# Kernel tuning notes

Hardware: AMD Instinct MI355X
Metric: run time of the kernel (lower is better)

## Reference

```python
import jax, jax.numpy as jnp
import numpy as np


def _leaky(x):
    return jnp.where(x >= 0, x, 0.01 * x)  # nn.LeakyReLU default slope


def _conv1x1(x, w):
    # x: [B, C, H, W], w: [O, C] (1x1 conv == per-pixel channel GEMM)
    return jnp.einsum('bchw,oc->bohw', x, w)


def setup_inputs() -> dict:
    key = jax.random.key(0)
    ks = jax.random.split(key, 12)

    def kaiming(k, o, c):  # kaiming_normal_ fan_out, relu gain, 1x1 kernel
        return jax.random.normal(k, (o, c), jnp.float32) * np.float32(np.sqrt(2.0 / o))

    lr_feature = jax.random.normal(ks[0], (1, 32, 256, 512), jnp.float32)
    hr_feature = jax.random.normal(ks[1], (1, 32, 512, 1024), jnp.float32)
    return {
        'lr_feature': lr_feature,
        'hr_feature': hr_feature,
        's1_w0': kaiming(ks[2], 128, 128),
        's1_w1': kaiming(ks[3], 64, 128),
        's1_w2': kaiming(ks[4], 32, 64),
        's1_w3': kaiming(ks[5], 16, 32),
        's1_w4': kaiming(ks[6], 8, 16),
        's1_w5': kaiming(ks[7], 1, 8),
        's2_w0': kaiming(ks[8], 3, 3),
        's2_w1': kaiming(ks[9], 2, 3),
        's2_w2': kaiming(ks[10], 1, 2),
        'fuse_w': jnp.ones((1, 2), jnp.float32),  # fuse weight initialized to 1
    }


def reference(lr_feature, hr_feature, s1_w0, s1_w1, s1_w2, s1_w3, s1_w4, s1_w5,
              s2_w0, s2_w1, s2_w2, fuse_w):
    scale = hr_feature.shape[-1] // lr_feature.shape[-1]  # static python int (=2, even)
    Hh, Wh = hr_feature.shape[-2], hr_feature.shape[-1]

    # nearest-neighbor upsample of lr_feature by `scale` (expand/view trick in torch)
    lr_up = jnp.repeat(jnp.repeat(lr_feature, scale, axis=2), scale, axis=3)

    # representation: [B, 128, Hh, Wh]
    rep = jnp.concatenate(
        [lr_up, hr_feature, lr_up * hr_feature, (lr_up - hr_feature) ** 2], axis=1)

    # similarity_measure1: 1x1-conv MLP chain 128->128->64->32->16->8->1
    o = _leaky(_conv1x1(rep, s1_w0))
    o = _leaky(_conv1x1(o, s1_w1))
    o = _leaky(_conv1x1(o, s1_w2))
    o = _leaky(_conv1x1(o, s1_w3))
    o = _conv1x1(o, s1_w4)
    weights1 = _conv1x1(o, s1_w5)  # [B, 1, Hh, Wh]

    # distance matrix (even-scale branch): 3 channels [dx, dy, norm]
    v = jnp.arange(-(scale // 2), scale // 2 + 1, dtype=jnp.float32)
    m = v.shape[0] // 2
    v = jnp.concatenate([v[:m], v[m + 1:]])  # drop center -> length `scale`
    d0 = jnp.broadcast_to(v[None, :], (scale, scale))
    dm = jnp.stack([d0, d0.T, jnp.sqrt(d0 ** 2 + d0.T ** 2)], axis=0)  # [3,s,s]
    dm = jnp.tile(dm, (1, Hh // scale, Wh // scale))[None]  # [1, 3, Hh, Wh]

    # similarity_measure2: 3->3->2->1
    w2 = _leaky(_conv1x1(dm, s2_w0))
    w2 = _leaky(_conv1x1(w2, s2_w1))
    weights2 = _conv1x1(w2, s2_w2)  # [1, 1, Hh, Wh]

    # fuse (weight forced non-negative via abs, as in forward's .data mutation)
    mapping = _conv1x1(jnp.concatenate([weights1, weights2], axis=1), jnp.abs(fuse_w))
    return mapping
```

## Files before the change

### kernel.cpp

```cpp
#include <hip/hip_runtime.h>

typedef short v8s __attribute__((ext_vector_type(8)));
typedef float v4f __attribute__((ext_vector_type(4)));
typedef unsigned v4u __attribute__((ext_vector_type(4)));

#define Wh   1024
#define Hh   512
#define HWh  (Wh * Hh)
#define Wlr  512
#define HWlr (Wlr * 256)
#define PAD  136
#define ITERS 8
#define NBLK  256

#define WFRAG_SHORTS (53 * 512)
#define ACT_SHORTS   (16 * PAD)
#define LDS_BYTES    ((WFRAG_SHORTS + 16 * ACT_SHORTS) * 2)

__device__ __forceinline__ unsigned short f2bf(float f) {
    union { float f; unsigned u; } v; v.f = f;
    unsigned r = v.u + 0x7FFFu + ((v.u >> 16) & 1u);
    return (unsigned short)(r >> 16);
}
__device__ __forceinline__ unsigned pk2(float a, float b) {
    union { float f; unsigned u; } ua, ub;
    ua.f = a; ub.f = b;
    return __builtin_amdgcn_perm(ub.u + 0x8000u, ua.u + 0x8000u, 0x07060302u);
}
__device__ __forceinline__ float leaky(float x) { return fmaxf(x, 0.01f * x); }

__global__ __launch_bounds__(1024, 4)
void cmfsm_kernel(const float* __restrict__ lr, const float* __restrict__ hr,
                  const float* __restrict__ w0g, const float* __restrict__ w1g,
                  const float* __restrict__ w2g, const float* __restrict__ w3g,
                  const float* __restrict__ w4g, const float* __restrict__ w5g,
                  const float* __restrict__ t0g, const float* __restrict__ t1g,
                  const float* __restrict__ t2g, const float* __restrict__ fwg,
                  float* __restrict__ out)
{
    extern __shared__ unsigned short smem[];
    unsigned short* wfrag = smem;
    unsigned short* actS  = smem + WFRAG_SHORTS;

    const int tid  = threadIdx.x;
    const int lane = tid & 63;
    const int wv   = tid >> 6;
    const int p    = lane & 15;
    const int q    = lane >> 4;

    for (int e = tid; e < 32 * 64; e += 1024) {
        int f = e >> 6, l = e & 63;
        int mt = f >> 2, ks = f & 3, pp = l & 15, qq = l >> 4;
        const float* src = w0g + (mt * 16 + pp) * 128 + ks * 32 + qq * 8;
        unsigned short* dst = wfrag + f * 512 + l * 8;
#pragma unroll
        for (int j = 0; j < 8; ++j) dst[j] = f2bf(src[j]);
    }
    if (tid < 16 * 64) {
        int f = tid >> 6, l = tid & 63;
        int mt = f >> 2, ks = f & 3, pp = l & 15, qq = l >> 4;
        const float* src = w1g + (mt * 16 + pp) * 128 + ks * 32 + qq * 8;
        unsigned short* dst = wfrag + (32 + f) * 512 + l * 8;
#pragma unroll
        for (int j = 0; j < 8; ++j) dst[j] = f2bf(src[j]);
    }
    if (tid < 4 * 64) {
        int f = tid >> 6, l = tid & 63;
        int mt = f >> 1, ks = f & 1, pp = l & 15, qq = l >> 4;
        const float* src = w2g + (mt * 16 + pp) * 64 + ks * 32 + qq * 8;
        unsigned short* dst = wfrag + (48 + f) * 512 + l * 8;
#pragma unroll
        for (int j = 0; j < 8; ++j) dst[j] = f2bf(src[j]);
    }
    if (tid < 64) {
        int l = tid;
        int pp = l & 15, qq = l >> 4;
        const float* src = w3g + pp * 32 + qq * 8;
        unsigned short* dst = wfrag + 52 * 512 + l * 8;
#pragma unroll
        for (int j = 0; j < 8; ++j) dst[j] = f2bf(src[j]);
    }

    float w45[4];
#pragma unroll
    for (int r = 0; r < 4; ++r) {
        float s = 0.f;
#pragma unroll
        for (int j = 0; j < 8; ++j) s += w5g[j] * w4g[j * 16 + q * 4 + r];
        w45[r] = s;
    }

    float w2t0, w2t1, w2t2, w2t3;
    {
        float tab[4];
#pragma unroll
        for (int yp = 0; yp < 2; ++yp)
#pragma unroll
            for (int xp = 0; xp < 2; ++xp) {
                float i0 = xp ? 1.f : -1.f;
                float i1 = yp ? 1.f : -1.f;
                float i2 = 1.41421356237309505f;
                float h0[3], h1[2];
                for (int o = 0; o < 3; ++o)
                    h0[o] = leaky(t0g[o*3+0]*i0 + t0g[o*3+1]*i1 + t0g[o*3+2]*i2);
                for (int o = 0; o < 2; ++o)
                    h1[o] = leaky(t1g[o*3+0]*h0[0] + t1g[o*3+1]*h0[1] + t1g[o*3+2]*h0[2]);
                tab[yp*2+xp] = t2g[0]*h1[0] + t2g[1]*h1[1];
            }
        w2t0 = tab[0]; w2t1 = tab[1]; w2t2 = tab[2]; w2t3 = tab[3];
    }
    const float fa = fabsf(fwg[0]);
    const float fb = fabsf(fwg[1]);

    __syncthreads();

    unsigned short* Arow = actS + wv * ACT_SHORTS + p * PAD;
    const unsigned short* ARq8 = Arow + q * 8;
    unsigned short* AWq4       = Arow + q * 4;
    const unsigned short* WL   = wfrag + lane * 8;

    const float* hrp[8];
    const float* lrp[8];
    {
        const int hbase = blockIdx.x * 2048 + wv * 16 + p;
        const int lbase = blockIdx.x * 512  + wv * 8  + (p >> 1);
#pragma unroll
        for (int j = 0; j < 8; ++j) {
            hrp[j] = hr + (size_t)(q * 8 + j) * HWh  + hbase;
            lrp[j] = lr + (size_t)(q * 8 + j) * HWlr + lbase;
        }
    }

    float h[8], l[8];
#pragma unroll
    for (int j = 0; j < 8; ++j) { h[j] = hrp[j][0]; l[j] = lrp[j][0]; }

#pragma unroll 1
    for (int t = 0; t < 2; ++t) {
#pragma unroll
        for (int s = 0; s < 4; ++s) {
            v4u bf0, bf1, bf2, bf3;
#pragma unroll
            for (int u = 0; u < 4; ++u) {
                float l0 = l[2*u], l1 = l[2*u+1];
                float h0 = h[2*u], h1 = h[2*u+1];
                bf0[u] = pk2(l0, l1);
                bf1[u] = pk2(h0, h1);
                bf2[u] = pk2(l0 * h0, l1 * h1);
                float d0 = l0 - h0, d1 = l1 - h1;
                bf3[u] = pk2(d0 * d0, d1 * d1);
            }
            v8s b0 = __builtin_bit_cast(v8s, bf0);
            v8s b1 = __builtin_bit_cast(v8s, bf1);
            v8s b2 = __builtin_bit_cast(v8s, bf2);
            v8s b3 = __builtin_bit_cast(v8s, bf3);

#pragma unroll
            for (int j = 0; j < 8; ++j) hrp[j] += 256;
            if (t == 0 || s < 3) {
                const int nlr = ((s + 1) & 3) * 128;
#pragma unroll
                for (int j = 0; j < 8; ++j) {
                    h[j] = hrp[j][0];
                    l[j] = lrp[j][nlr];
                }
            }

#pragma unroll
            for (int half = 0; half < 2; ++half) {
                v4f acc[4];
#pragma unroll
                for (int m2 = 0; m2 < 4; ++m2) acc[m2] = (v4f){0.f, 0.f, 0.f, 0.f};
#pragma unroll
                for (int ks = 0; ks < 4; ++ks) {
                    v8s b = (ks == 0) ? b0 : (ks == 1) ? b1 : (ks == 2) ? b2 : b3;
#pragma unroll
                    for (int m2 = 0; m2 < 4; ++m2) {
                        const int mt = half * 4 + m2;
                        v8s a = *(const v8s*)(WL + (mt * 4 + ks) * 512);
                        acc[m2] = __builtin_amdgcn_mfma_f32_16x16x32_bf16(a, b, acc[m2], 0, 0, 0);
                    }
                }
#pragma unroll
                for (int m2 = 0; m2 < 4; ++m2) {
                    const int mt = half * 4 + m2;
                    uint2 v;
                    v.x = pk2(leaky(acc[m2][0]), leaky(acc[m2][1]));
                    v.y = pk2(leaky(acc[m2][2]), leaky(acc[m2][3]));
                    *(uint2*)(AWq4 + mt * 16) = v;
                }
            }

            {
                v4f acc1[4];
#pragma unroll
                for (int mt = 0; mt < 4; ++mt) acc1[mt] = (v4f){0.f, 0.f, 0.f, 0.f};
#pragma unroll
                for (int ks = 0; ks < 4; ++ks) {
                    v8s b = *(const v8s*)(ARq8 + ks * 32);
#pragma unroll
                    for (int mt = 0; mt < 4; ++mt) {
                        v8s a = *(const v8s*)(WL + (32 + mt * 4 + ks) * 512);
                        acc1[mt] = __builtin_amdgcn_mfma_f32_16x16x32_bf16(a, b, acc1[mt], 0, 0, 0);
                    }
                }
#pragma unroll
                for (int mt = 0; mt < 4; ++mt) {
                    uint2 v;
                    v.x = pk2(leaky(acc1[mt][0]), leaky(acc1[mt][1]));
                    v.y = pk2(leaky(acc1[mt][2]), leaky(acc1[mt][3]));
                    *(uint2*)(AWq4 + mt * 16) = v;
                }
            }

            {
                v4f acc2[2];
#pragma unroll
                for (int mt = 0; mt < 2; ++mt) acc2[mt] = (v4f){0.f, 0.f, 0.f, 0.f};
#pragma unroll
                for (int ks = 0; ks < 2; ++ks) {
                    v8s b = *(const v8s*)(ARq8 + ks * 32);
#pragma unroll
                    for (int mt = 0; mt < 2; ++mt) {
                        v8s a = *(const v8s*)(WL + (48 + mt * 2 + ks) * 512);
                        acc2[mt] = __builtin_amdgcn_mfma_f32_16x16x32_bf16(a, b, acc2[mt], 0, 0, 0);
                    }
                }
#pragma unroll
                for (int mt = 0; mt < 2; ++mt) {
                    uint2 v;
                    v.x = pk2(leaky(acc2[mt][0]), leaky(acc2[mt][1]));
                    v.y = pk2(leaky(acc2[mt][2]), leaky(acc2[mt][3]));
                    *(uint2*)(AWq4 + mt * 16) = v;
                }
            }

            {
                v8s b = *(const v8s*)(ARq8);
                v8s a = *(const v8s*)(WL + 52 * 512);
                v4f acc3 = __builtin_amdgcn_mfma_f32_16x16x32_bf16(a, b, (v4f){0.f, 0.f, 0.f, 0.f}, 0, 0, 0);

                float part = 0.f;
#pragma unroll
                for (int r = 0; r < 4; ++r) part += w45[r] * leaky(acc3[r]);
                part += __shfl_xor(part, 16, 64);
                part += __shfl_xor(part, 32, 64);

                if (q == 0) {
                    const float w2v = t ? ((p & 1) ? w2t3 : w2t2)
                                        : ((p & 1) ? w2t1 : w2t0);
                    const int gidx = blockIdx.x * 2048 + (t * 4 + s) * 256 + wv * 16 + p;
                    out[gidx] = fa * part + fb * w2v;
                }
            }
        }
    }
}

extern "C" void kernel_launch(void* const* d_in, const int* in_sizes, int n_in,
                              void* d_out, int out_size, void* d_ws, size_t ws_size,
                              hipStream_t stream) {
    const float* lr  = (const float*)d_in[0];
    const float* hr  = (const float*)d_in[1];
    const float* w0g = (const float*)d_in[2];
    const float* w1g = (const float*)d_in[3];
    const float* w2g = (const float*)d_in[4];
    const float* w3g = (const float*)d_in[5];
    const float* w4g = (const float*)d_in[6];
    const float* w5g = (const float*)d_in[7];
    const float* t0g = (const float*)d_in[8];
    const float* t1g = (const float*)d_in[9];
    const float* t2g = (const float*)d_in[10];
    const float* fwg = (const float*)d_in[11];
    float* out = (float*)d_out;

    hipLaunchKernelGGL(cmfsm_kernel, dim3(NBLK), dim3(1024), LDS_BYTES, stream,
                       lr, hr, w0g, w1g, w2g, w3g, w4g, w5g, t0g, t1g, t2g, fwg, out);
}
```

Measured before the change: 149.6 us.

## Chain MLP layers through registers by permuting weight K-order instead of LDS

Removes the per-wave LDS activation staging buffer. MFMA accumulator outputs are packed directly into the B operands of the next layer, and the weight fragments for layers 1-3 are loaded with a permuted K index so the register layout of the outputs lines up. The layer-3 weight fragment is also hoisted into a register before the loop. This eliminates LDS writes and reads, and the waits between layers, at the cost of more live registers (8 accumulators for layer 0), which could add spill or scheduling pressure.

```diff
diff --git a/kernel.cpp b/kernel.cpp
--- a/kernel.cpp
+++ b/kernel.cpp
@@ -9,13 +9,11 @@
 #define HWh  (Wh * Hh)
 #define Wlr  512
 #define HWlr (Wlr * 256)
-#define PAD  136
 #define ITERS 8
 #define NBLK  256
 
 #define WFRAG_SHORTS (53 * 512)
-#define ACT_SHORTS   (16 * PAD)
-#define LDS_BYTES    ((WFRAG_SHORTS + 16 * ACT_SHORTS) * 2)
+#define LDS_BYTES    (WFRAG_SHORTS * 2)
 
 __device__ __forceinline__ unsigned short f2bf(float f) {
     union { float f; unsigned u; } v; v.f = f;
@@ -28,6 +26,15 @@
     return __builtin_amdgcn_perm(ub.u + 0x8000u, ua.u + 0x8000u, 0x07060302u);
 }
 __device__ __forceinline__ float leaky(float x) { return fmaxf(x, 0.01f * x); }
+
+__device__ __forceinline__ v8s relay(const v4f& e, const v4f& o) {
+    v4u w;
+    w[0] = pk2(leaky(e[0]), leaky(e[1]));
+    w[1] = pk2(leaky(e[2]), leaky(e[3]));
+    w[2] = pk2(leaky(o[0]), leaky(o[1]));
+    w[3] = pk2(leaky(o[2]), leaky(o[3]));
+    return __builtin_bit_cast(v8s, w);
+}
 
 __global__ __launch_bounds__(1024, 4)
 void cmfsm_kernel(const float* __restrict__ lr, const float* __restrict__ hr,
@@ -40,7 +47,6 @@
 {
     extern __shared__ unsigned short smem[];
     unsigned short* wfrag = smem;
-    unsigned short* actS  = smem + WFRAG_SHORTS;
 
     const int tid  = threadIdx.x;
     const int lane = tid & 63;
@@ -59,26 +65,29 @@
     if (tid < 16 * 64) {
         int f = tid >> 6, l = tid & 63;
         int mt = f >> 2, ks = f & 3, pp = l & 15, qq = l >> 4;
-        const float* src = w1g + (mt * 16 + pp) * 128 + ks * 32 + qq * 8;
+        const float* srcrow = w1g + (mt * 16 + pp) * 128;
         unsigned short* dst = wfrag + (32 + f) * 512 + l * 8;
 #pragma unroll
-        for (int j = 0; j < 8; ++j) dst[j] = f2bf(src[j]);
+        for (int j = 0; j < 8; ++j)
+            dst[j] = f2bf(srcrow[ks * 32 + ((j >> 2) << 4) + qq * 4 + (j & 3)]);
     }
     if (tid < 4 * 64) {
         int f = tid >> 6, l = tid & 63;
         int mt = f >> 1, ks = f & 1, pp = l & 15, qq = l >> 4;
-        const float* src = w2g + (mt * 16 + pp) * 64 + ks * 32 + qq * 8;
+        const float* srcrow = w2g + (mt * 16 + pp) * 64;
         unsigned short* dst = wfrag + (48 + f) * 512 + l * 8;
 #pragma unroll
-        for (int j = 0; j < 8; ++j) dst[j] = f2bf(src[j]);
+        for (int j = 0; j < 8; ++j)
+            dst[j] = f2bf(srcrow[ks * 32 + ((j >> 2) << 4) + qq * 4 + (j & 3)]);
     }
     if (tid < 64) {
         int l = tid;
         int pp = l & 15, qq = l >> 4;
-        const float* src = w3g + pp * 32 + qq * 8;
+        const float* srcrow = w3g + pp * 32;
         unsigned short* dst = wfrag + 52 * 512 + l * 8;
 #pragma unroll
-        for (int j = 0; j < 8; ++j) dst[j] = f2bf(src[j]);
+        for (int j = 0; j < 8; ++j)
+            dst[j] = f2bf(srcrow[((j >> 2) << 4) + qq * 4 + (j & 3)]);
     }
 
     float w45[4];
@@ -114,10 +123,7 @@
 
     __syncthreads();
 
-    unsigned short* Arow = actS + wv * ACT_SHORTS + p * PAD;
-    const unsigned short* ARq8 = Arow + q * 8;
-    unsigned short* AWq4       = Arow + q * 4;
-    const unsigned short* WL   = wfrag + lane * 8;
+    const unsigned short* WL = wfrag + lane * 8;
 
     const float* hrp[8];
     const float* lrp[8];
@@ -130,6 +136,8 @@
             lrp[j] = lr + (size_t)(q * 8 + j) * HWlr + lbase;
         }
     }
+
+    const v8s a3 = *(const v8s*)(WL + 52 * 512);
 
     float h[8], l[8];
 #pragma unroll
@@ -166,79 +174,54 @@
                 }
             }
 
-#pragma unroll
-            for (int half = 0; half < 2; ++half) {
-                v4f acc[4];
-#pragma unroll
-                for (int m2 = 0; m2 < 4; ++m2) acc[m2] = (v4f){0.f, 0.f, 0.f, 0.f};
-#pragma unroll
-                for (int ks = 0; ks < 4; ++ks) {
-                    v8s b = (ks == 0) ? b0 : (ks == 1) ? b1 : (ks == 2) ? b2 : b3;
-#pragma unroll
-                    for (int m2 = 0; m2 < 4; ++m2) {
-                        const int mt = half * 4 + m2;
-                        v8s a = *(const v8s*)(WL + (mt * 4 + ks) * 512);
-                        acc[m2] = __builtin_amdgcn_mfma_f32_16x16x32_bf16(a, b, acc[m2], 0, 0, 0);
-                    }
-                }
-#pragma unroll
-                for (int m2 = 0; m2 < 4; ++m2) {
-                    const int mt = half * 4 + m2;
-                    uint2 v;
-                    v.x = pk2(leaky(acc[m2][0]), leaky(acc[m2][1]));
-                    v.y = pk2(leaky(acc[m2][2]), leaky(acc[m2][3]));
-                    *(uint2*)(AWq4 + mt * 16) = v;
+            v4f acc0[8];
+#pragma unroll
+            for (int mt = 0; mt < 8; ++mt) acc0[mt] = (v4f){0.f, 0.f, 0.f, 0.f};
+#pragma unroll
+            for (int ks = 0; ks < 4; ++ks) {
+                v8s b = (ks == 0) ? b0 : (ks == 1) ? b1 : (ks == 2) ? b2 : b3;
+#pragma unroll
+                for (int mt = 0; mt < 8; ++mt) {
+                    v8s a = *(const v8s*)(WL + (mt * 4 + ks) * 512);
+                    acc0[mt] = __builtin_amdgcn_mfma_f32_16x16x32_bf16(a, b, acc0[mt], 0, 0, 0);
+                }
+            }
+
+            v8s c1[4];
+#pragma unroll
+            for (int ks = 0; ks < 4; ++ks) c1[ks] = relay(acc0[2*ks], acc0[2*ks+1]);
+
+            v4f acc1[4];
+#pragma unroll
+            for (int mt = 0; mt < 4; ++mt) acc1[mt] = (v4f){0.f, 0.f, 0.f, 0.f};
+#pragma unroll
+            for (int ks = 0; ks < 4; ++ks) {
+#pragma unroll
+                for (int mt = 0; mt < 4; ++mt) {
+                    v8s a = *(const v8s*)(WL + (32 + mt * 4 + ks) * 512);
+                    acc1[mt] = __builtin_amdgcn_mfma_f32_16x16x32_bf16(a, c1[ks], acc1[mt], 0, 0, 0);
+                }
+            }
+
+            v8s c2[2];
+#pragma unroll
+            for (int ks = 0; ks < 2; ++ks) c2[ks] = relay(acc1[2*ks], acc1[2*ks+1]);
+
+            v4f acc2[2];
+#pragma unroll
+            for (int mt = 0; mt < 2; ++mt) acc2[mt] = (v4f){0.f, 0.f, 0.f, 0.f};
+#pragma unroll
+            for (int ks = 0; ks < 2; ++ks) {
+#pragma unroll
+                for (int mt = 0; mt < 2; ++mt) {
+                    v8s a = *(const v8s*)(WL + (48 + mt * 2 + ks) * 512);
+                    acc2[mt] = __builtin_amdgcn_mfma_f32_16x16x32_bf16(a, c2[ks], acc2[mt], 0, 0, 0);
                 }
             }
 
             {
-                v4f acc1[4];
-#pragma unroll
-                for (int mt = 0; mt < 4; ++mt) acc1[mt] = (v4f){0.f, 0.f, 0.f, 0.f};
-#pragma unroll
-                for (int ks = 0; ks < 4; ++ks) {
-                    v8s b = *(const v8s*)(ARq8 + ks * 32);
-#pragma unroll
-                    for (int mt = 0; mt < 4; ++mt) {
-                        v8s a = *(const v8s*)(WL + (32 + mt * 4 + ks) * 512);
-                        acc1[mt] = __builtin_amdgcn_mfma_f32_16x16x32_bf16(a, b, acc1[mt], 0, 0, 0);
-                    }
-                }
-#pragma unroll
-                for (int mt = 0; mt < 4; ++mt) {
-                    uint2 v;
-                    v.x = pk2(leaky(acc1[mt][0]), leaky(acc1[mt][1]));
-                    v.y = pk2(leaky(acc1[mt][2]), leaky(acc1[mt][3]));
-                    *(uint2*)(AWq4 + mt * 16) = v;
-                }
-            }
-
-            {
-                v4f acc2[2];
-#pragma unroll
-                for (int mt = 0; mt < 2; ++mt) acc2[mt] = (v4f){0.f, 0.f, 0.f, 0.f};
-#pragma unroll
-                for (int ks = 0; ks < 2; ++ks) {
-                    v8s b = *(const v8s*)(ARq8 + ks * 32);
-#pragma unroll
-                    for (int mt = 0; mt < 2; ++mt) {
-                        v8s a = *(const v8s*)(WL + (48 + mt * 2 + ks) * 512);
-                        acc2[mt] = __builtin_amdgcn_mfma_f32_16x16x32_bf16(a, b, acc2[mt], 0, 0, 0);
-                    }
-                }
-#pragma unroll
-                for (int mt = 0; mt < 2; ++mt) {
-                    uint2 v;
-                    v.x = pk2(leaky(acc2[mt][0]), leaky(acc2[mt][1]));
-                    v.y = pk2(leaky(acc2[mt][2]), leaky(acc2[mt][3]));
-                    *(uint2*)(AWq4 + mt * 16) = v;
-                }
-            }
-
-            {
-                v8s b = *(const v8s*)(ARq8);
-                v8s a = *(const v8s*)(WL + 52 * 512);
-                v4f acc3 = __builtin_amdgcn_mfma_f32_16x16x32_bf16(a, b, (v4f){0.f, 0.f, 0.f, 0.f}, 0, 0, 0);
+                v8s c3 = relay(acc2[0], acc2[1]);
+                v4f acc3 = __builtin_amdgcn_mfma_f32_16x16x32_bf16(a3, c3, (v4f){0.f, 0.f, 0.f, 0.f}, 0, 0, 0);
 
                 float part = 0.f;
 #pragma unroll
```

New measurement: 459.9 us. 3.07x slower.
